# Kernel optimization log

Measured on AMD Instinct MI355X. Metric: run time of the kernel, lower is better.

The kernel has to match this reference:

```python
import jax, jax.numpy as jnp
import numpy as np

N = 100000
E = 1600000
IN_DIM = 128
HID = 64
HEADS = 4
OUT = HID // HEADS  # 16
LAYERS = 3
NEG_SLOPE = 0.2
LN_EPS = 1e-5


def setup_inputs() -> dict:
    key = jax.random.key(0)
    ks = jax.random.split(key, 12)
    x = jax.random.normal(ks[0], (N, IN_DIM), dtype=jnp.float32)
    edge_index = jax.random.randint(ks[1], (2, E), 0, N, dtype=jnp.int32)
    s = 0.05
    Win = jax.random.normal(ks[2], (IN_DIM, HID), dtype=jnp.float32) * s
    bin_ = jnp.zeros((HID,), dtype=jnp.float32)
    Wg = jax.random.normal(ks[3], (LAYERS, HID, HEADS * OUT), dtype=jnp.float32) * s
    att_src = jax.random.normal(ks[4], (LAYERS, HEADS, OUT), dtype=jnp.float32) * s
    att_dst = jax.random.normal(ks[5], (LAYERS, HEADS, OUT), dtype=jnp.float32) * s
    bg = jnp.zeros((LAYERS, HID), dtype=jnp.float32)
    ln_g = jnp.ones((LAYERS, HID), dtype=jnp.float32)
    ln_b = jnp.zeros((LAYERS, HID), dtype=jnp.float32)
    Wout = jax.random.normal(ks[6], (HID, 1), dtype=jnp.float32) * s
    bout = jnp.zeros((1,), dtype=jnp.float32)
    return {"x": x, "edge_index": edge_index, "Win": Win, "bin_": bin_,
            "Wg": Wg, "att_src": att_src, "att_dst": att_dst, "bg": bg,
            "ln_g": ln_g, "ln_b": ln_b, "Wout": Wout, "bout": bout}


def _gat_layer(x, src, dst, W, a_s, a_d, b):
    # x: [N, HID]; linear transform then split heads
    h = (x @ W).reshape(N, HEADS, OUT)                       # [N,H,C]
    alpha_s = jnp.einsum('nhc,hc->nh', h, a_s)               # [N,H]
    alpha_d = jnp.einsum('nhc,hc->nh', h, a_d)               # [N,H]
    e = alpha_s[src] + alpha_d[dst]                          # [E',H]
    e = jnp.where(e > 0, e, NEG_SLOPE * e)                   # LeakyReLU(0.2)
    # segment softmax over destination node
    m = jax.ops.segment_max(e, dst, num_segments=N)          # [N,H]
    ee = jnp.exp(e - m[dst])
    z = jax.ops.segment_sum(ee, dst, num_segments=N)         # [N,H]
    alpha = ee / (z[dst] + 1e-16)                            # [E',H]
    msg = alpha[:, :, None] * h[src]                         # [E',H,C]
    out = jax.ops.segment_sum(msg, dst, num_segments=N)      # [N,H,C]
    return out.reshape(N, HID) + b


def _layer_norm(x, g, b):
    mu = jnp.mean(x, axis=-1, keepdims=True)
    var = jnp.mean(jnp.square(x - mu), axis=-1, keepdims=True)
    return (x - mu) * jax.lax.rsqrt(var + LN_EPS) * g + b


def reference(x, edge_index, Win, bin_, Wg, att_src, att_dst, bg, ln_g, ln_b, Wout, bout):
    # add self loops (PyG GATConv default)
    loops = jnp.arange(N, dtype=edge_index.dtype)
    src = jnp.concatenate([edge_index[0], loops])
    dst = jnp.concatenate([edge_index[1], loops])
    h = jax.nn.relu(x @ Win + bin_)                          # input_proj + ReLU
    for i in range(LAYERS):
        res = h
        h = _gat_layer(h, src, dst, Wg[i], att_src[i], att_dst[i], bg[i])
        h = _layer_norm(h, ln_g[i], ln_b[i])
        h = jax.nn.relu(h)
        h = h + res                                          # dropout is identity in eval
    out = h @ Wout + bout                                    # [N,1]
    return out.reshape(-1)
```

## Files before the change

kernel.cpp:

```cpp
#include <hip/hip_runtime.h>
#include <hip/hip_bf16.h>

#define N_NODES 100000
#define E_EDGES 1600000
#define IN_DIM  128
#define HID     64
#define HEADS   4
#define NEG_SLOPE 0.2f
#define LN_EPS  1e-5f
#define LOG2E   1.4426950408889634f

#define BUCK_SHIFT 7
#define NODES_PER_BUCK 128
#define NBUCK ((N_NODES + NODES_PER_BUCK - 1) / NODES_PER_BUCK)
#define NBUCK_PAD 1024
#define PART_CHUNK 8192
#define HIST_BLOCKS 256

typedef float f2v __attribute__((ext_vector_type(2)));

__device__ __forceinline__ f2v unp2(unsigned u) {
    f2v r; r.x = __uint_as_float(u << 16); r.y = __uint_as_float(u & 0xffff0000u); return r;
}
__device__ __forceinline__ unsigned packbf2(float a, float b) {
    unsigned ua = __float_as_uint(a), ub = __float_as_uint(b);
    ua += 0x7fffu + ((ua >> 16) & 1u);
    ub += 0x7fffu + ((ub >> 16) & 1u);
    return (ua >> 16) | (ub & 0xffff0000u);
}
__device__ __forceinline__ float lrexp2(float e) {
    return __builtin_amdgcn_exp2f(fmaxf(e, NEG_SLOPE * e));
}

__global__ __launch_bounds__(256) void k_in_proj(
        const float* __restrict__ x, const float* __restrict__ W,
        const float* __restrict__ bias, float* __restrict__ h) {
    __shared__ float Xs[32][132];
    __shared__ float Ws[64][64];
    int t = threadIdx.x;
    int base = blockIdx.x * 32;
    const float4* X4 = (const float4*)(x + (size_t)base * IN_DIM);
    #pragma unroll
    for (int i = 0; i < 4; ++i) {
        int f = t + 256 * i;
        ((float4*)&Xs[f >> 5][0])[f & 31] = X4[f];
    }
    const float4* W4 = (const float4*)W;
    float4* Ws4 = (float4*)&Ws[0][0];
    #pragma unroll
    for (int i = 0; i < 4; ++i) Ws4[t + 256 * i] = W4[t + 256 * i];
    __syncthreads();
    int r = t >> 4;
    int c = (t & 15) * 4;
    float4 bb = *(const float4*)(bias + c);
    float4 acc0 = bb, acc1 = bb;
    #pragma unroll 8
    for (int k = 0; k < 64; ++k) {
        float a0 = Xs[r][k];
        float a1 = Xs[r + 16][k];
        float4 b = *(const float4*)&Ws[k][c];
        acc0.x += a0 * b.x; acc0.y += a0 * b.y; acc0.z += a0 * b.z; acc0.w += a0 * b.w;
        acc1.x += a1 * b.x; acc1.y += a1 * b.y; acc1.z += a1 * b.z; acc1.w += a1 * b.w;
    }
    __syncthreads();
    #pragma unroll
    for (int i = 0; i < 4; ++i) Ws4[t + 256 * i] = W4[1024 + t + 256 * i];
    __syncthreads();
    #pragma unroll 8
    for (int k = 0; k < 64; ++k) {
        float a0 = Xs[r][64 + k];
        float a1 = Xs[r + 16][64 + k];
        float4 b = *(const float4*)&Ws[k][c];
        acc0.x += a0 * b.x; acc0.y += a0 * b.y; acc0.z += a0 * b.z; acc0.w += a0 * b.w;
        acc1.x += a1 * b.x; acc1.y += a1 * b.y; acc1.z += a1 * b.z; acc1.w += a1 * b.w;
    }
    acc0.x = fmaxf(acc0.x, 0.f); acc0.y = fmaxf(acc0.y, 0.f);
    acc0.z = fmaxf(acc0.z, 0.f); acc0.w = fmaxf(acc0.w, 0.f);
    acc1.x = fmaxf(acc1.x, 0.f); acc1.y = fmaxf(acc1.y, 0.f);
    acc1.z = fmaxf(acc1.z, 0.f); acc1.w = fmaxf(acc1.w, 0.f);
    *(float4*)(h + (size_t)(base + r) * HID + c) = acc0;
    *(float4*)(h + (size_t)(base + r + 16) * HID + c) = acc1;
}

__global__ __launch_bounds__(256) void k_gat_lin(
        const float* __restrict__ h, const float* __restrict__ W,
        const float* __restrict__ as_w, const float* __restrict__ ad_w,
        unsigned* __restrict__ hlb, float* __restrict__ as_o, float* __restrict__ ad_o) {
    __shared__ float Xs[32][68];
    __shared__ float Ws[64][64];
    int t = threadIdx.x;
    const float4* W4 = (const float4*)W;
    float4* Ws4 = (float4*)&Ws[0][0];
    #pragma unroll
    for (int i = 0; i < 4; ++i) Ws4[t + 256 * i] = W4[t + 256 * i];
    int base = blockIdx.x * 32;
    const float4* X4 = (const float4*)(h + (size_t)base * HID);
    #pragma unroll
    for (int i = 0; i < 2; ++i) {
        int f = t + 256 * i;
        ((float4*)&Xs[f >> 4][0])[f & 15] = X4[f];
    }
    __syncthreads();
    int r = t >> 4;
    int c = (t & 15) * 4;
    float4 acc0 = {0.f, 0.f, 0.f, 0.f}, acc1 = {0.f, 0.f, 0.f, 0.f};
    #pragma unroll 8
    for (int k = 0; k < 64; ++k) {
        float a0 = Xs[r][k];
        float a1 = Xs[r + 16][k];
        float4 b = *(const float4*)&Ws[k][c];
        acc0.x += a0 * b.x; acc0.y += a0 * b.y; acc0.z += a0 * b.z; acc0.w += a0 * b.w;
        acc1.x += a1 * b.x; acc1.y += a1 * b.y; acc1.z += a1 * b.z; acc1.w += a1 * b.w;
    }
    uint2 p0, p1;
    p0.x = packbf2(acc0.x, acc0.y); p0.y = packbf2(acc0.z, acc0.w);
    p1.x = packbf2(acc1.x, acc1.y); p1.y = packbf2(acc1.z, acc1.w);
    ((uint2*)hlb)[(size_t)(base + r) * 16 + (c >> 2)] = p0;
    ((uint2*)hlb)[(size_t)(base + r + 16) * 16 + (c >> 2)] = p1;
    float4 A = *(const float4*)(as_w + c);
    float4 D = *(const float4*)(ad_w + c);
    A.x *= LOG2E; A.y *= LOG2E; A.z *= LOG2E; A.w *= LOG2E;
    D.x *= LOG2E; D.y *= LOG2E; D.z *= LOG2E; D.w *= LOG2E;
    float s0 = acc0.x * A.x + acc0.y * A.y + acc0.z * A.z + acc0.w * A.w;
    float d0 = acc0.x * D.x + acc0.y * D.y + acc0.z * D.z + acc0.w * D.w;
    float s1 = acc1.x * A.x + acc1.y * A.y + acc1.z * A.z + acc1.w * A.w;
    float d1 = acc1.x * D.x + acc1.y * D.y + acc1.z * D.z + acc1.w * D.w;
    #pragma unroll
    for (int off = 1; off < 4; off <<= 1) {
        s0 += __shfl_xor(s0, off); d0 += __shfl_xor(d0, off);
        s1 += __shfl_xor(s1, off); d1 += __shfl_xor(d1, off);
    }
    if ((t & 3) == 0) {
        int head = (t & 15) >> 2;
        as_o[(size_t)(base + r) * HEADS + head] = s0;
        ad_o[(size_t)(base + r) * HEADS + head] = d0;
        as_o[(size_t)(base + r + 16) * HEADS + head] = s1;
        ad_o[(size_t)(base + r + 16) * HEADS + head] = d1;
    }
}

__global__ __launch_bounds__(256) void k_bhist_scan(
        const int* __restrict__ dstp, int* __restrict__ bcnt,
        int* __restrict__ done, int* __restrict__ bbase, int* __restrict__ bcur) {
    __shared__ int c[NBUCK_PAD];
    __shared__ int tsum[256];
    __shared__ int lastFlag;
    int t = threadIdx.x;
    for (int i = t; i < NBUCK_PAD; i += 256) c[i] = 0;
    __syncthreads();
    for (int i = blockIdx.x * 256 + t; i < E_EDGES; i += gridDim.x * 256)
        atomicAdd(&c[dstp[i] >> BUCK_SHIFT], 1);
    __syncthreads();
    for (int i = t; i < NBUCK_PAD; i += 256) {
        int v = c[i];
        if (v) atomicAdd(bcnt + i, v);
    }
    __threadfence();
    if (t == 0) lastFlag = (atomicAdd(done, 1) == (int)gridDim.x - 1);
    __syncthreads();
    if (!lastFlag) return;
    int v0 = bcnt[t * 4 + 0], v1 = bcnt[t * 4 + 1];
    int v2 = bcnt[t * 4 + 2], v3 = bcnt[t * 4 + 3];
    int local = v0 + v1 + v2 + v3;
    tsum[t] = local;
    __syncthreads();
    for (int off = 1; off < 256; off <<= 1) {
        int u = (t >= off) ? tsum[t - off] : 0;
        __syncthreads();
        tsum[t] += u;
        __syncthreads();
    }
    int p = tsum[t] - local;
    bbase[t * 4 + 0] = p; bcur[t * 4 + 0] = p; p += v0;
    bbase[t * 4 + 1] = p; bcur[t * 4 + 1] = p; p += v1;
    bbase[t * 4 + 2] = p; bcur[t * 4 + 2] = p; p += v2;
    bbase[t * 4 + 3] = p; bcur[t * 4 + 3] = p; p += v3;
    if (t == 255) bbase[NBUCK_PAD] = p;
}

__global__ __launch_bounds__(1024) void k_part(const int* __restrict__ srcp,
                                               const int* __restrict__ dstp,
                                               int* __restrict__ bcur,
                                               unsigned* __restrict__ ebuf) {
    __shared__ int cnt[NBUCK_PAD];
    __shared__ int gbase[NBUCK_PAD];
    int t = threadIdx.x;
    cnt[t] = 0;
    int e0 = blockIdx.x * PART_CHUNK;
    int e1 = min(e0 + PART_CHUNK, E_EDGES);
    __syncthreads();
    for (int i = e0 + t; i < e1; i += 1024)
        atomicAdd(&cnt[dstp[i] >> BUCK_SHIFT], 1);
    __syncthreads();
    {
        int c = cnt[t];
        gbase[t] = c ? atomicAdd(bcur + t, c) : 0;
        cnt[t] = 0;
    }
    __syncthreads();
    for (int i = e0 + t; i < e1; i += 1024) {
        int d = dstp[i];
        int b = d >> BUCK_SHIFT;
        int pos = gbase[b] + atomicAdd(&cnt[b], 1);
        ebuf[pos] = (unsigned)srcp[i] | ((unsigned)(d & 127) << 17);
    }
}

__global__ __launch_bounds__(256) void k_fin(const int* __restrict__ bbase,
                                             const unsigned* __restrict__ ebuf,
                                             int* __restrict__ row,
                                             int* __restrict__ ssrc) {
    __shared__ int cnt[NODES_PER_BUCK];
    __shared__ int sc[NODES_PER_BUCK];
    __shared__ int rbase[NODES_PER_BUCK];
    int t = threadIdx.x;
    int b = blockIdx.x;
    int start = bbase[b], end = bbase[b + 1];
    int nb0 = b << BUCK_SHIFT;
    if (t < NODES_PER_BUCK) cnt[t] = 0;
    __syncthreads();
    for (int i = start + t; i < end; i += 256)
        atomicAdd(&cnt[ebuf[i] >> 17], 1);
    __syncthreads();
    if (t < NODES_PER_BUCK) sc[t] = cnt[t];
    __syncthreads();
    for (int off = 1; off < NODES_PER_BUCK; off <<= 1) {
        int v = (t < NODES_PER_BUCK && t >= off) ? sc[t - off] : 0;
        __syncthreads();
        if (t < NODES_PER_BUCK) sc[t] += v;
        __syncthreads();
    }
    if (t < NODES_PER_BUCK) {
        int rb = start + sc[t] - cnt[t];
        rbase[t] = rb;
        int n = nb0 + t;
        if (n < N_NODES) row[n] = rb;
        cnt[t] = 0;
    }
    if (b == NBUCK - 1 && t == 0) row[N_NODES] = E_EDGES;
    __syncthreads();
    for (int i = start + t; i < end; i += 256) {
        unsigned p = ebuf[i];
        int l = (int)(p >> 17);
        int slot = rbase[l] + atomicAdd(&cnt[l], 1);
        ssrc[slot] = (int)(p & 0x1FFFFu);
    }
}

__global__ __launch_bounds__(256) void k_gat_agg(
        const int* __restrict__ row, const int* __restrict__ ssrc,
        const float* __restrict__ as_, const float* __restrict__ ad_,
        const unsigned* __restrict__ hlb, const float* __restrict__ hres,
        const float* __restrict__ bg, const float* __restrict__ g,
        const float* __restrict__ b, float* __restrict__ hout,
        const float* __restrict__ Wout, const float* __restrict__ bout,
        float* __restrict__ out, int last) {
    int gid = blockIdx.x * blockDim.x + threadIdx.x;
    int lane = threadIdx.x & 63;
    int grp = lane >> 3;
    int q   = lane & 7;
    int n = (gid >> 6) * 8 + grp;
    if (n >= N_NODES) return;
    int head = q >> 1;
    const char* hlbc = (const char*)hlb;
    const char* asc  = (const char*)as_;
    unsigned nb = (unsigned)n;
    unsigned qb = (unsigned)q * 16u;
    unsigned hb = (unsigned)head * 4u;
    float adh = *(const float*)((const char*)ad_ + (nb * 16u + hb));
    float w = lrexp2(*(const float*)(asc + (nb * 16u + hb)) + adh);
    f2v w2; w2.x = w; w2.y = w;
    uint4 u = *(const uint4*)(hlbc + (nb * 128u + qb));
    f2v acc0 = w2 * unp2(u.x);
    f2v acc1 = w2 * unp2(u.y);
    f2v acc2 = w2 * unp2(u.z);
    f2v acc3 = w2 * unp2(u.w);
    float z = w;
    int j = row[n];
    int jend = row[n + 1];
    for (; j + 3 < jend; j += 4) {
        unsigned s0 = (unsigned)ssrc[j],     s1 = (unsigned)ssrc[j + 1];
        unsigned s2 = (unsigned)ssrc[j + 2], s3 = (unsigned)ssrc[j + 3];
        float wa = lrexp2(*(const float*)(asc + (s0 * 16u + hb)) + adh);
        float wb = lrexp2(*(const float*)(asc + (s1 * 16u + hb)) + adh);
        float wc = lrexp2(*(const float*)(asc + (s2 * 16u + hb)) + adh);
        float wd = lrexp2(*(const float*)(asc + (s3 * 16u + hb)) + adh);
        uint4 ua = *(const uint4*)(hlbc + (s0 * 128u + qb));
        uint4 ub = *(const uint4*)(hlbc + (s1 * 128u + qb));
        uint4 uc = *(const uint4*)(hlbc + (s2 * 128u + qb));
        uint4 ud = *(const uint4*)(hlbc + (s3 * 128u + qb));
        f2v wa2; wa2.x = wa; wa2.y = wa;
        f2v wb2; wb2.x = wb; wb2.y = wb;
        f2v wc2; wc2.x = wc; wc2.y = wc;
        f2v wd2; wd2.x = wd; wd2.y = wd;
        acc0 += wa2 * unp2(ua.x); acc1 += wa2 * unp2(ua.y);
        acc2 += wa2 * unp2(ua.z); acc3 += wa2 * unp2(ua.w);
        acc0 += wb2 * unp2(ub.x); acc1 += wb2 * unp2(ub.y);
        acc2 += wb2 * unp2(ub.z); acc3 += wb2 * unp2(ub.w);
        acc0 += wc2 * unp2(uc.x); acc1 += wc2 * unp2(uc.y);
        acc2 += wc2 * unp2(uc.z); acc3 += wc2 * unp2(uc.w);
        acc0 += wd2 * unp2(ud.x); acc1 += wd2 * unp2(ud.y);
        acc2 += wd2 * unp2(ud.z); acc3 += wd2 * unp2(ud.w);
        z += wa + wb + wc + wd;
    }
    for (; j < jend; ++j) {
        unsigned s0 = (unsigned)ssrc[j];
        float wa = lrexp2(*(const float*)(asc + (s0 * 16u + hb)) + adh);
        uint4 ua = *(const uint4*)(hlbc + (s0 * 128u + qb));
        f2v wa2; wa2.x = wa; wa2.y = wa;
        acc0 += wa2 * unp2(ua.x); acc1 += wa2 * unp2(ua.y);
        acc2 += wa2 * unp2(ua.z); acc3 += wa2 * unp2(ua.w);
        z += wa;
    }
    float rz = 1.f / (z + 1e-16f);
    float4 bg0 = ((const float4*)bg)[2 * q];
    float4 bg1 = ((const float4*)bg)[2 * q + 1];
    float v[8];
    v[0] = acc0.x * rz + bg0.x; v[1] = acc0.y * rz + bg0.y;
    v[2] = acc1.x * rz + bg0.z; v[3] = acc1.y * rz + bg0.w;
    v[4] = acc2.x * rz + bg1.x; v[5] = acc2.y * rz + bg1.y;
    v[6] = acc3.x * rz + bg1.z; v[7] = acc3.y * rz + bg1.w;
    float ssum = 0.f;
    #pragma unroll
    for (int i = 0; i < 8; ++i) ssum += v[i];
    #pragma unroll
    for (int off = 1; off < 8; off <<= 1) ssum += __shfl_xor(ssum, off);
    float mu = ssum * (1.f / 64.f);
    float vs = 0.f;
    #pragma unroll
    for (int i = 0; i < 8; ++i) { v[i] -= mu; vs += v[i] * v[i]; }
    #pragma unroll
    for (int off = 1; off < 8; off <<= 1) vs += __shfl_xor(vs, off);
    float rstd = rsqrtf(vs * (1.f / 64.f) + LN_EPS);
    float4 g0 = ((const float4*)g)[2 * q];
    float4 g1 = ((const float4*)g)[2 * q + 1];
    float4 b0 = ((const float4*)b)[2 * q];
    float4 b1 = ((const float4*)b)[2 * q + 1];
    float4 h0 = ((const float4*)hres)[(size_t)n * 16 + 2 * q];
    float4 h1 = ((const float4*)hres)[(size_t)n * 16 + 2 * q + 1];
    float y[8];
    y[0] = fmaxf(v[0] * rstd * g0.x + b0.x, 0.f) + h0.x;
    y[1] = fmaxf(v[1] * rstd * g0.y + b0.y, 0.f) + h0.y;
    y[2] = fmaxf(v[2] * rstd * g0.z + b0.z, 0.f) + h0.z;
    y[3] = fmaxf(v[3] * rstd * g0.w + b0.w, 0.f) + h0.w;
    y[4] = fmaxf(v[4] * rstd * g1.x + b1.x, 0.f) + h1.x;
    y[5] = fmaxf(v[5] * rstd * g1.y + b1.y, 0.f) + h1.y;
    y[6] = fmaxf(v[6] * rstd * g1.z + b1.z, 0.f) + h1.z;
    y[7] = fmaxf(v[7] * rstd * g1.w + b1.w, 0.f) + h1.w;
    if (!last) {
        float4 o0; o0.x = y[0]; o0.y = y[1]; o0.z = y[2]; o0.w = y[3];
        float4 o1; o1.x = y[4]; o1.y = y[5]; o1.z = y[6]; o1.w = y[7];
        ((float4*)hout)[(size_t)n * 16 + 2 * q] = o0;
        ((float4*)hout)[(size_t)n * 16 + 2 * q + 1] = o1;
    } else {
        float4 w0 = ((const float4*)Wout)[2 * q];
        float4 w1 = ((const float4*)Wout)[2 * q + 1];
        float pp = y[0] * w0.x + y[1] * w0.y + y[2] * w0.z + y[3] * w0.w
                 + y[4] * w1.x + y[5] * w1.y + y[6] * w1.z + y[7] * w1.w;
        #pragma unroll
        for (int off = 1; off < 8; off <<= 1) pp += __shfl_xor(pp, off);
        if (q == 0) out[n] = pp + bout[0];
    }
}

extern "C" void kernel_launch(void* const* d_in, const int* in_sizes, int n_in,
                              void* d_out, int out_size, void* d_ws, size_t ws_size,
                              hipStream_t stream) {
    const float* x     = (const float*)d_in[0];
    const int*   ei    = (const int*)  d_in[1];
    const float* Win   = (const float*)d_in[2];
    const float* bin_  = (const float*)d_in[3];
    const float* Wg    = (const float*)d_in[4];
    const float* att_s = (const float*)d_in[5];
    const float* att_d = (const float*)d_in[6];
    const float* bg    = (const float*)d_in[7];
    const float* lng   = (const float*)d_in[8];
    const float* lnb   = (const float*)d_in[9];
    const float* Wout  = (const float*)d_in[10];
    const float* bout  = (const float*)d_in[11];
    float* out = (float*)d_out;

    float* hA   = (float*)d_ws;
    float* hC   = hA + (size_t)N_NODES * 64;
    unsigned* hlb = (unsigned*)(hC + (size_t)N_NODES * 64);
    float* as_  = (float*)(hlb + (size_t)N_NODES * 32);
    float* ad_  = as_ + (size_t)N_NODES * 4;
    int* row    = (int*)(ad_ + (size_t)N_NODES * 4);
    int* bcnt   = row + (N_NODES + 1);
    int* done   = bcnt + NBUCK_PAD;
    int* bbase  = done + 1;
    int* bcur   = bbase + (NBUCK_PAD + 1);
    int* ssrc   = bcur + NBUCK_PAD;
    unsigned* ebuf = (unsigned*)(ssrc + E_EDGES);

    const int* srcp = ei;
    const int* dstp = ei + E_EDGES;

    hipMemsetAsync(bcnt, 0, (NBUCK_PAD + 1) * sizeof(int), stream);
    k_bhist_scan<<<HIST_BLOCKS, 256, 0, stream>>>(dstp, bcnt, done, bbase, bcur);
    k_part<<<(E_EDGES + PART_CHUNK - 1) / PART_CHUNK, 1024, 0, stream>>>(srcp, dstp, bcur, ebuf);
    k_fin<<<NBUCK, 256, 0, stream>>>(bbase, ebuf, row, ssrc);

    k_in_proj<<<N_NODES / 32, 256, 0, stream>>>(x, Win, bin_, hA);

    const int aggBlocks = (N_NODES + 31) / 32;
    for (int L = 0; L < 3; ++L) {
        k_gat_lin<<<N_NODES / 32, 256, 0, stream>>>(hA, Wg + L * 64 * 64,
                                            att_s + L * 64, att_d + L * 64,
                                            hlb, as_, ad_);
        k_gat_agg<<<aggBlocks, 256, 0, stream>>>(row, ssrc, as_, ad_, hlb, hA,
                                                 bg + L * 64, lng + L * 64, lnb + L * 64,
                                                 hC, Wout, bout, out, (L == 2) ? 1 : 0);
        float* t = hA; hA = hC; hC = t;
    }
}
```

Before: 295.7 us.

## Fuse GAT linear projection into input projection and aggregation epilogue

Removes the separate k_gat_lin kernel. The first layer's linear transform and attention scores are computed inside the input projection kernel, and each later layer's transform is computed in the epilogue of the previous layer's aggregation kernel. The epilogue uses warp shuffles and a shared-memory weight tile, and the bf16 features and attention scores are double-buffered across layers. This saves launches and one read of the hidden state per layer. In exchange the aggregation kernel gets extra shared memory, a block-wide sync and a 64-step FMA loop, which may lower occupancy for the memory-bound gather.

Measured after the change: 296.5 us. About the same (+0.3%).

```diff
diff --git a/kernel.cpp b/kernel.cpp
--- a/kernel.cpp
+++ b/kernel.cpp
@@ -32,9 +32,13 @@
     return __builtin_amdgcn_exp2f(fmaxf(e, NEG_SLOPE * e));
 }
 
-__global__ __launch_bounds__(256) void k_in_proj(
+__global__ __launch_bounds__(256) void k_in_proj_fused(
         const float* __restrict__ x, const float* __restrict__ W,
-        const float* __restrict__ bias, float* __restrict__ h) {
+        const float* __restrict__ bias,
+        const float* __restrict__ W2g, const float* __restrict__ as_w,
+        const float* __restrict__ ad_w,
+        float* __restrict__ h, unsigned* __restrict__ hlb,
+        float* __restrict__ as_o, float* __restrict__ ad_o) {
     __shared__ float Xs[32][132];
     __shared__ float Ws[64][64];
     int t = threadIdx.x;
@@ -80,51 +84,36 @@
     acc1.z = fmaxf(acc1.z, 0.f); acc1.w = fmaxf(acc1.w, 0.f);
     *(float4*)(h + (size_t)(base + r) * HID + c) = acc0;
     *(float4*)(h + (size_t)(base + r + 16) * HID + c) = acc1;
-}
-
-__global__ __launch_bounds__(256) void k_gat_lin(
-        const float* __restrict__ h, const float* __restrict__ W,
-        const float* __restrict__ as_w, const float* __restrict__ ad_w,
-        unsigned* __restrict__ hlb, float* __restrict__ as_o, float* __restrict__ ad_o) {
-    __shared__ float Xs[32][68];
-    __shared__ float Ws[64][64];
-    int t = threadIdx.x;
-    const float4* W4 = (const float4*)W;
-    float4* Ws4 = (float4*)&Ws[0][0];
-    #pragma unroll
-    for (int i = 0; i < 4; ++i) Ws4[t + 256 * i] = W4[t + 256 * i];
-    int base = blockIdx.x * 32;
-    const float4* X4 = (const float4*)(h + (size_t)base * HID);
-    #pragma unroll
-    for (int i = 0; i < 2; ++i) {
-        int f = t + 256 * i;
-        ((float4*)&Xs[f >> 4][0])[f & 15] = X4[f];
-    }
-    __syncthreads();
-    int r = t >> 4;
-    int c = (t & 15) * 4;
-    float4 acc0 = {0.f, 0.f, 0.f, 0.f}, acc1 = {0.f, 0.f, 0.f, 0.f};
+    __syncthreads();
+    float (*H2)[68] = (float(*)[68])Xs;
+    *(float4*)&H2[r][c] = acc0;
+    *(float4*)&H2[r + 16][c] = acc1;
+    const float4* W24 = (const float4*)W2g;
+    #pragma unroll
+    for (int i = 0; i < 4; ++i) Ws4[t + 256 * i] = W24[t + 256 * i];
+    __syncthreads();
+    float4 s0v = {0.f,0.f,0.f,0.f}, s1v = {0.f,0.f,0.f,0.f};
     #pragma unroll 8
     for (int k = 0; k < 64; ++k) {
-        float a0 = Xs[r][k];
-        float a1 = Xs[r + 16][k];
+        float a0 = H2[r][k];
+        float a1 = H2[r + 16][k];
         float4 b = *(const float4*)&Ws[k][c];
-        acc0.x += a0 * b.x; acc0.y += a0 * b.y; acc0.z += a0 * b.z; acc0.w += a0 * b.w;
-        acc1.x += a1 * b.x; acc1.y += a1 * b.y; acc1.z += a1 * b.z; acc1.w += a1 * b.w;
+        s0v.x += a0 * b.x; s0v.y += a0 * b.y; s0v.z += a0 * b.z; s0v.w += a0 * b.w;
+        s1v.x += a1 * b.x; s1v.y += a1 * b.y; s1v.z += a1 * b.z; s1v.w += a1 * b.w;
     }
     uint2 p0, p1;
-    p0.x = packbf2(acc0.x, acc0.y); p0.y = packbf2(acc0.z, acc0.w);
-    p1.x = packbf2(acc1.x, acc1.y); p1.y = packbf2(acc1.z, acc1.w);
+    p0.x = packbf2(s0v.x, s0v.y); p0.y = packbf2(s0v.z, s0v.w);
+    p1.x = packbf2(s1v.x, s1v.y); p1.y = packbf2(s1v.z, s1v.w);
     ((uint2*)hlb)[(size_t)(base + r) * 16 + (c >> 2)] = p0;
     ((uint2*)hlb)[(size_t)(base + r + 16) * 16 + (c >> 2)] = p1;
     float4 A = *(const float4*)(as_w + c);
     float4 D = *(const float4*)(ad_w + c);
     A.x *= LOG2E; A.y *= LOG2E; A.z *= LOG2E; A.w *= LOG2E;
     D.x *= LOG2E; D.y *= LOG2E; D.z *= LOG2E; D.w *= LOG2E;
-    float s0 = acc0.x * A.x + acc0.y * A.y + acc0.z * A.z + acc0.w * A.w;
-    float d0 = acc0.x * D.x + acc0.y * D.y + acc0.z * D.z + acc0.w * D.w;
-    float s1 = acc1.x * A.x + acc1.y * A.y + acc1.z * A.z + acc1.w * A.w;
-    float d1 = acc1.x * D.x + acc1.y * D.y + acc1.z * D.z + acc1.w * D.w;
+    float s0 = s0v.x * A.x + s0v.y * A.y + s0v.z * A.z + s0v.w * A.w;
+    float d0 = s0v.x * D.x + s0v.y * D.y + s0v.z * D.z + s0v.w * D.w;
+    float s1 = s1v.x * A.x + s1v.y * A.y + s1v.z * A.z + s1v.w * A.w;
+    float d1 = s1v.x * D.x + s1v.y * D.y + s1v.z * D.z + s1v.w * D.w;
     #pragma unroll
     for (int off = 1; off < 4; off <<= 1) {
         s0 += __shfl_xor(s0, off); d0 += __shfl_xor(d0, off);
@@ -253,10 +242,22 @@
         const unsigned* __restrict__ hlb, const float* __restrict__ hres,
         const float* __restrict__ bg, const float* __restrict__ g,
         const float* __restrict__ b, float* __restrict__ hout,
+        const float* __restrict__ W2g, const float* __restrict__ as_w2,
+        const float* __restrict__ ad_w2, unsigned* __restrict__ hlb_out,
+        float* __restrict__ as_out, float* __restrict__ ad_out,
         const float* __restrict__ Wout, const float* __restrict__ bout,
         float* __restrict__ out, int last) {
-    int gid = blockIdx.x * blockDim.x + threadIdx.x;
-    int lane = threadIdx.x & 63;
+    __shared__ float W2s[64][64];
+    int t = threadIdx.x;
+    if (!last) {
+        const float4* W24 = (const float4*)W2g;
+        float4* W2s4 = (float4*)&W2s[0][0];
+        #pragma unroll
+        for (int i = 0; i < 4; ++i) W2s4[t + 256 * i] = W24[t + 256 * i];
+    }
+    __syncthreads();
+    int gid = blockIdx.x * blockDim.x + t;
+    int lane = t & 63;
     int grp = lane >> 3;
     int q   = lane & 7;
     int n = (gid >> 6) * 8 + grp;
@@ -352,6 +353,39 @@
         float4 o1; o1.x = y[4]; o1.y = y[5]; o1.z = y[6]; o1.w = y[7];
         ((float4*)hout)[(size_t)n * 16 + 2 * q] = o0;
         ((float4*)hout)[(size_t)n * 16 + 2 * q + 1] = o1;
+        f2v hl0 = {0.f,0.f}, hl1 = {0.f,0.f}, hl2 = {0.f,0.f}, hl3 = {0.f,0.f};
+        int lbase = lane & 56;
+        int q8 = q * 8;
+        #pragma unroll
+        for (int k = 0; k < 64; ++k) {
+            float yk = __shfl(y[k & 7], lbase + (k >> 3));
+            float4 w0 = *(const float4*)&W2s[k][q8];
+            float4 w1 = *(const float4*)&W2s[k][q8 + 4];
+            hl0.x += yk * w0.x; hl0.y += yk * w0.y;
+            hl1.x += yk * w0.z; hl1.y += yk * w0.w;
+            hl2.x += yk * w1.x; hl2.y += yk * w1.y;
+            hl3.x += yk * w1.z; hl3.y += yk * w1.w;
+        }
+        uint4 pk;
+        pk.x = packbf2(hl0.x, hl0.y);
+        pk.y = packbf2(hl1.x, hl1.y);
+        pk.z = packbf2(hl2.x, hl2.y);
+        pk.w = packbf2(hl3.x, hl3.y);
+        ((uint4*)hlb_out)[(size_t)n * 8 + q] = pk;
+        float4 A0 = ((const float4*)as_w2)[2 * q];
+        float4 A1 = ((const float4*)as_w2)[2 * q + 1];
+        float4 D0 = ((const float4*)ad_w2)[2 * q];
+        float4 D1 = ((const float4*)ad_w2)[2 * q + 1];
+        float s = (hl0.x * A0.x + hl0.y * A0.y + hl1.x * A0.z + hl1.y * A0.w
+                 + hl2.x * A1.x + hl2.y * A1.y + hl3.x * A1.z + hl3.y * A1.w) * LOG2E;
+        float d = (hl0.x * D0.x + hl0.y * D0.y + hl1.x * D0.z + hl1.y * D0.w
+                 + hl2.x * D1.x + hl2.y * D1.y + hl3.x * D1.z + hl3.y * D1.w) * LOG2E;
+        s += __shfl_xor(s, 1);
+        d += __shfl_xor(d, 1);
+        if (!(q & 1)) {
+            as_out[(size_t)n * 4 + (q >> 1)] = s;
+            ad_out[(size_t)n * 4 + (q >> 1)] = d;
+        }
     } else {
         float4 w0 = ((const float4*)Wout)[2 * q];
         float4 w1 = ((const float4*)Wout)[2 * q + 1];
@@ -380,18 +414,25 @@
     const float* bout  = (const float*)d_in[11];
     float* out = (float*)d_out;
 
-    float* hA   = (float*)d_ws;
-    float* hC   = hA + (size_t)N_NODES * 64;
-    unsigned* hlb = (unsigned*)(hC + (size_t)N_NODES * 64);
-    float* as_  = (float*)(hlb + (size_t)N_NODES * 32);
-    float* ad_  = as_ + (size_t)N_NODES * 4;
-    int* row    = (int*)(ad_ + (size_t)N_NODES * 4);
-    int* bcnt   = row + (N_NODES + 1);
-    int* done   = bcnt + NBUCK_PAD;
-    int* bbase  = done + 1;
-    int* bcur   = bbase + (NBUCK_PAD + 1);
-    int* ssrc   = bcur + NBUCK_PAD;
+    float* hA    = (float*)d_ws;
+    float* hC    = hA + (size_t)N_NODES * 64;
+    unsigned* hlb0 = (unsigned*)(hC + (size_t)N_NODES * 64);
+    unsigned* hlb1 = hlb0 + (size_t)N_NODES * 32;
+    float* as0   = (float*)(hlb1 + (size_t)N_NODES * 32);
+    float* ad0   = as0 + (size_t)N_NODES * 4;
+    float* as1   = ad0 + (size_t)N_NODES * 4;
+    float* ad1   = as1 + (size_t)N_NODES * 4;
+    int* row     = (int*)(ad1 + (size_t)N_NODES * 4);
+    int* bcnt    = row + (N_NODES + 1);
+    int* done    = bcnt + NBUCK_PAD;
+    int* bbase   = done + 1;
+    int* bcur    = bbase + (NBUCK_PAD + 1);
+    int* ssrc    = bcur + NBUCK_PAD;
     unsigned* ebuf = (unsigned*)(ssrc + E_EDGES);
+
+    unsigned* hlbs[2] = {hlb0, hlb1};
+    float* ass[2] = {as0, as1};
+    float* ads[2] = {ad0, ad1};
 
     const int* srcp = ei;
     const int* dstp = ei + E_EDGES;
@@ -401,16 +442,21 @@
     k_part<<<(E_EDGES + PART_CHUNK - 1) / PART_CHUNK, 1024, 0, stream>>>(srcp, dstp, bcur, ebuf);
     k_fin<<<NBUCK, 256, 0, stream>>>(bbase, ebuf, row, ssrc);
 
-    k_in_proj<<<N_NODES / 32, 256, 0, stream>>>(x, Win, bin_, hA);
+    k_in_proj_fused<<<N_NODES / 32, 256, 0, stream>>>(
+        x, Win, bin_, Wg, att_s, att_d, hA, hlb0, as0, ad0);
 
     const int aggBlocks = (N_NODES + 31) / 32;
     for (int L = 0; L < 3; ++L) {
-        k_gat_lin<<<N_NODES / 32, 256, 0, stream>>>(hA, Wg + L * 64 * 64,
-                                            att_s + L * 64, att_d + L * 64,
-                                            hlb, as_, ad_);
-        k_gat_agg<<<aggBlocks, 256, 0, stream>>>(row, ssrc, as_, ad_, hlb, hA,
-                                                 bg + L * 64, lng + L * 64, lnb + L * 64,
-                                                 hC, Wout, bout, out, (L == 2) ? 1 : 0);
-        float* t = hA; hA = hC; hC = t;
-    }
-}
+        int cur = L & 1, nxt = cur ^ 1;
+        int last = (L == 2) ? 1 : 0;
+        const float* W2g = last ? Wg : (Wg + (L + 1) * 64 * 64);
+        const float* aw2 = last ? att_s : (att_s + (L + 1) * 64);
+        const float* dw2 = last ? att_d : (att_d + (L + 1) * 64);
+        k_gat_agg<<<aggBlocks, 256, 0, stream>>>(
+            row, ssrc, ass[cur], ads[cur], hlbs[cur], hA,
+            bg + L * 64, lng + L * 64, lnb + L * 64, hC,
+            W2g, aw2, dw2, hlbs[nxt], ass[nxt], ads[nxt],
+            Wout, bout, out, last);
+        float* tp = hA; hA = hC; hC = tp;
+    }
+}
```
